# Kernel optimization log

Hardware: AMD Instinct MI355X
Metric: run time of the kernel (lower is better)

The kernel has to match this reference:

```python
import jax, jax.numpy as jnp
import numpy as np

B, N, C = 128, 512, 512  # batch, num_proposals, hidden_dim
K = 3                    # kernel_size
EPS = 1e-5               # LayerNorm eps (torch default)


def setup_inputs() -> dict:
    key = jax.random.key(0)
    k1, k2, k3, k4 = jax.random.split(key, 4)
    query = jax.random.normal(k1, (B, N, C), dtype=jnp.float32)
    value = jax.random.normal(k2, (B, N, C), dtype=jnp.float32)
    # nn.Linear(C, N+K): store transposed weight [C, N+K] for x @ W
    lim = 1.0 / np.sqrt(C)
    W_lin = jax.random.uniform(k3, (C, N + K), minval=-lim, maxval=lim, dtype=jnp.float32)
    b_lin = jax.random.uniform(k4, (N + K,), minval=-lim, maxval=lim, dtype=jnp.float32)
    gamma = jnp.ones((C,), dtype=jnp.float32)
    beta = jnp.zeros((C,), dtype=jnp.float32)
    return {"query": query, "value": value, "W_lin": W_lin, "b_lin": b_lin,
            "gamma": gamma, "beta": beta}


def reference(query, value, W_lin, b_lin, gamma, beta):
    # dynamic weights: [B, N, N+K]
    dy = jnp.einsum('bnc,ck->bnk', query, W_lin) + b_lin
    dw = dy[..., :K]          # depthwise kernel  [B, N, 3]
    pw = dy[..., K:]          # pointwise weights [B, N(out), N(in)]
    # depthwise conv1d along C, groups=N, padding='same' (cross-correlation)
    vp = jnp.pad(value, ((0, 0), (0, 0), (1, 1)))
    depth = (dw[..., 0:1] * vp[..., 0:C]
             + dw[..., 1:2] * vp[..., 1:C + 1]
             + dw[..., 2:3] * vp[..., 2:C + 2])
    depth = jax.nn.relu(depth)
    # pointwise (1x1) conv across proposals: out[b,m,c] = sum_n pw[b,m,n] * depth[b,n,c]
    out = jnp.einsum('bmn,bnc->bmc', pw, depth)
    # LayerNorm over last dim C
    mu = jnp.mean(out, axis=-1, keepdims=True)
    var = jnp.mean(jnp.square(out - mu), axis=-1, keepdims=True)
    return (out - mu) * jax.lax.rsqrt(var + EPS) * gamma + beta
```

## Files before the change

### kernel.cpp

```cpp
#include <hip/hip_runtime.h>
#include <hip/hip_bf16.h>

typedef unsigned short u16;
typedef unsigned int u32;
typedef __attribute__((ext_vector_type(8))) short short8;
typedef __attribute__((ext_vector_type(8))) unsigned short ushort8;
typedef __attribute__((ext_vector_type(4))) float f32x4;

#define AS1 __attribute__((address_space(1)))
#define AS3 __attribute__((address_space(3)))

#define Bb_ 128
#define Nn_ 512
#define Cc_ 512
#define NK_ 515

__device__ __forceinline__ u16 f2bf(float f) {
    union { float f; u32 i; } t; t.f = f;
    u32 x = t.i;
    u32 r = (x + 0x7fffu + ((x >> 16) & 1u)) >> 16;
    return (u16)r;
}

#define ROWS_PER_WAVE 32
__global__ void prep_kernel(const float* __restrict__ q, const float* __restrict__ W,
                            const float* __restrict__ bl,
                            u16* __restrict__ qbf, float* __restrict__ dw) {
    __shared__ float wc[3][512];
    int tid = threadIdx.x;
    for (int idx = tid; idx < 3 * 512; idx += 256) {
        int j = idx >> 9, c = idx & 511;
        wc[j][c] = W[c * NK_ + j];
    }
    __syncthreads();

    int w = tid >> 6, l = tid & 63;
    int c0 = l * 8;
    float w0[8], w1[8], w2[8];
#pragma unroll
    for (int e = 0; e < 8; e++) {
        w0[e] = wc[0][c0 + e];
        w1[e] = wc[1][c0 + e];
        w2[e] = wc[2][c0 + e];
    }
    float bl0 = bl[0], bl1 = bl[1], bl2 = bl[2];

    size_t row0 = (size_t)blockIdx.x * (4 * ROWS_PER_WAVE) + (size_t)w * ROWS_PER_WAVE;
#pragma unroll 2
    for (int rr = 0; rr < ROWS_PER_WAVE; rr++) {
        size_t row = row0 + rr;
        const float* qr = q + row * Cc_;
        f32x4 x0 = *(const f32x4*)(qr + c0);
        f32x4 x1 = *(const f32x4*)(qr + c0 + 4);
        float xf[8] = {x0[0], x0[1], x0[2], x0[3], x1[0], x1[1], x1[2], x1[3]};
        ushort8 y;
        float s0 = 0.f, s1 = 0.f, s2 = 0.f;
#pragma unroll
        for (int e = 0; e < 8; e++) {
            float qf = xf[e];
            y[e] = f2bf(qf);
            s0 += qf * w0[e];
            s1 += qf * w1[e];
            s2 += qf * w2[e];
        }
        *(ushort8*)(qbf + row * Cc_ + c0) = y;
#pragma unroll
        for (int off = 32; off > 0; off >>= 1) {
            s0 += __shfl_xor(s0, off);
            s1 += __shfl_xor(s1, off);
            s2 += __shfl_xor(s2, off);
        }
        if (l == 0) {
            dw[row * 3 + 0] = s0 + bl0;
            dw[row * 3 + 1] = s1 + bl1;
            dw[row * 3 + 2] = s2 + bl2;
        }
    }
}

__global__ void wt_kernel(const float* __restrict__ W, u16* __restrict__ WT) {
    int n = blockIdx.y;
    int c = blockIdx.x * 256 + threadIdx.x;
    WT[n * Cc_ + c] = f2bf(W[c * NK_ + n + 3]);
}

__global__ void depthT_kernel(const float* __restrict__ val, const float* __restrict__ dw,
                              u16* __restrict__ dT) {
    __shared__ float vt[64][67];
    __shared__ float dws[64][3];
    int b = blockIdx.z;
    int c0 = blockIdx.x * 64;
    int n0 = blockIdx.y * 64;
    int tid = threadIdx.x;

    const float* vbase = val + ((size_t)b * Nn_ + n0) * Cc_;
    for (int idx = tid; idx < 64 * 66; idx += 256) {
        int r = idx / 66, cc = idx % 66;
        int c = c0 - 1 + cc;
        float x = 0.f;
        if (c >= 0 && c < Cc_) x = vbase[(size_t)r * Cc_ + c];
        vt[r][cc] = x;
    }
    if (tid < 192) {
        int r = tid / 3, j = tid % 3;
        dws[r][j] = dw[((size_t)b * Nn_ + n0 + r) * 3 + j];
    }
    __syncthreads();

    int nn = tid & 63;
    int ccb = tid >> 6;
    u16* out = dT + ((size_t)b * Cc_ + c0) * Nn_ + n0;
    float d0 = dws[nn][0], d1 = dws[nn][1], d2 = dws[nn][2];
#pragma unroll
    for (int p = 0; p < 16; p++) {
        int cc = ccb + p * 4;
        float x = d0 * vt[nn][cc] + d1 * vt[nn][cc + 1] + d2 * vt[nn][cc + 2];
        x = x > 0.f ? x : 0.f;
        out[(size_t)cc * Nn_ + nn] = f2bf(x);
    }
}

template <int BIAS, int F32OUT>
__global__ __launch_bounds__(256, 2) void gemm_bt(const u16* __restrict__ A,
                                                  const u16* __restrict__ Bt,
                                                  void* __restrict__ Outv,
                                                  const float* __restrict__ bias,
                                                  long sA, long sB, long sO) {
    __shared__ __align__(16) u16 lA[128 * 32];
    __shared__ __align__(16) u16 lB[128 * 32];

    int b = blockIdx.y;
    int tileM = blockIdx.x >> 2;
    int tileN = blockIdx.x & 3;
    const u16* Ab = A + (size_t)b * sA + (size_t)tileM * 128 * 512;
    const u16* Bbp = Bt + (size_t)b * sB + (size_t)tileN * 128 * 512;

    int tid = threadIdx.x, w = tid >> 6, l = tid & 63;
    int rsub = l >> 2;
    int csub = l & 3;
    int wm = w & 1, wn = w >> 1;
    int m_off = wm * 64, n_off = wn * 64;
    int row_l = l & 15, quad = l >> 4;

    f32x4 acc[4][4];
#pragma unroll
    for (int i = 0; i < 4; i++)
#pragma unroll
        for (int j = 0; j < 4; j++) acc[i][j] = (f32x4){0.f, 0.f, 0.f, 0.f};

    for (int kt = 0; kt < 16; kt++) {
        __syncthreads();
        int kof = kt * 32;
#pragma unroll
        for (int j = 0; j < 2; j++) {
            int seg = w * 2 + j;
            int r = seg * 16 + rsub;
            const u16* gA = Ab + (size_t)r * 512 + kof + csub * 8;
            __builtin_amdgcn_global_load_lds((const AS1 u32*)gA,
                                             (AS3 u32*)&lA[seg * 512], 16, 0, 0);
            const u16* gB = Bbp + (size_t)r * 512 + kof + csub * 8;
            __builtin_amdgcn_global_load_lds((const AS1 u32*)gB,
                                             (AS3 u32*)&lB[seg * 512], 16, 0, 0);
        }
        __syncthreads();

        short8 aF[4], bF[4];
#pragma unroll
        for (int i = 0; i < 4; i++)
            aF[i] = *(const short8*)&lA[(m_off + i * 16 + row_l) * 32 + quad * 8];
#pragma unroll
        for (int j = 0; j < 4; j++)
            bF[j] = *(const short8*)&lB[(n_off + j * 16 + row_l) * 32 + quad * 8];

#pragma unroll
        for (int i = 0; i < 4; i++)
#pragma unroll
            for (int j = 0; j < 4; j++)
                acc[i][j] = __builtin_amdgcn_mfma_f32_16x16x32_bf16(aF[i], bF[j], acc[i][j], 0, 0, 0);
    }

#pragma unroll
    for (int i = 0; i < 4; i++) {
#pragma unroll
        for (int j = 0; j < 4; j++) {
            int gn = n_off + j * 16 + row_l;
            float bv = 0.f;
            if (BIAS) bv = bias[tileN * 128 + gn];
#pragma unroll
            for (int r = 0; r < 4; r++) {
                int gm = m_off + i * 16 + quad * 4 + r;
                float vv = acc[i][j][r] + bv;
                size_t idx = (size_t)b * sO + (size_t)tileM * 128 * 512 + tileN * 128 +
                             (size_t)gm * 512 + gn;
                if (F32OUT) ((float*)Outv)[idx] = vv;
                else        ((u16*)Outv)[idx] = f2bf(vv);
            }
        }
    }
}

__global__ void ln_kernel(float* __restrict__ out, const float* __restrict__ gamma,
                          const float* __restrict__ beta) {
    int tid = threadIdx.x, w = tid >> 6, l = tid & 63;
    size_t row = (size_t)blockIdx.x * 4 + w;
    float* p = out + row * Cc_ + l * 8;
    f32x4 x0 = *(const f32x4*)p;
    f32x4 x1 = *(const f32x4*)(p + 4);
    float xf[8] = {x0[0], x0[1], x0[2], x0[3], x1[0], x1[1], x1[2], x1[3]};
    float s = 0.f, ss = 0.f;
#pragma unroll
    for (int e = 0; e < 8; e++) {
        s += xf[e];
        ss += xf[e] * xf[e];
    }
#pragma unroll
    for (int off = 32; off > 0; off >>= 1) {
        s += __shfl_xor(s, off);
        ss += __shfl_xor(ss, off);
    }
    float mu = s * (1.f / 512.f);
    float var = ss * (1.f / 512.f) - mu * mu;
    float rs = rsqrtf(var + 1e-5f);
    f32x4 g0 = *(const f32x4*)(gamma + l * 8);
    f32x4 g1 = *(const f32x4*)(gamma + l * 8 + 4);
    f32x4 b0 = *(const f32x4*)(beta + l * 8);
    f32x4 b1 = *(const f32x4*)(beta + l * 8 + 4);
    float gf[8] = {g0[0], g0[1], g0[2], g0[3], g1[0], g1[1], g1[2], g1[3]};
    float bf[8] = {b0[0], b0[1], b0[2], b0[3], b1[0], b1[1], b1[2], b1[3]};
    f32x4 y0, y1;
#pragma unroll
    for (int e = 0; e < 8; e++) {
        float v = (xf[e] - mu) * rs * gf[e] + bf[e];
        if (e < 4) y0[e] = v; else y1[e - 4] = v;
    }
    *(f32x4*)p = y0;
    *(f32x4*)(p + 4) = y1;
}

extern "C" void kernel_launch(void* const* d_in, const int* in_sizes, int n_in,
                              void* d_out, int out_size, void* d_ws, size_t ws_size,
                              hipStream_t stream) {
    const float* q     = (const float*)d_in[0];
    const float* v     = (const float*)d_in[1];
    const float* W     = (const float*)d_in[2];
    const float* bl    = (const float*)d_in[3];
    const float* gamma = (const float*)d_in[4];
    const float* beta  = (const float*)d_in[5];

    char* ws = (char*)d_ws;
    u16*   WT  = (u16*)ws;
    float* dw  = (float*)(ws + 524288);
    u16*   pw  = (u16*)(ws + 1310720);
    u16*   dT  = (u16*)(ws + 68419584);
    float* out = (float*)d_out;
    u16*   qbf = (u16*)d_out;

    prep_kernel<<<dim3((Bb_ * Nn_) / (4 * ROWS_PER_WAVE)), 256, 0, stream>>>(q, W, bl, qbf, dw);
    wt_kernel<<<dim3(2, 512), 256, 0, stream>>>(W, WT);
    depthT_kernel<<<dim3(8, 8, Bb_), 256, 0, stream>>>(v, dw, dT);

    gemm_bt<1, 0><<<dim3(16, Bb_), 256, 0, stream>>>(qbf, WT, pw, bl + 3,
                                                     (long)Nn_ * Cc_, 0L, (long)Nn_ * Nn_);
    gemm_bt<0, 1><<<dim3(16, Bb_), 256, 0, stream>>>(pw, dT, out, nullptr,
                                                     (long)Nn_ * Nn_, (long)Cc_ * Nn_, (long)Nn_ * Cc_);

    ln_kernel<<<dim3((Bb_ * Nn_) / 4), 256, 0, stream>>>(out, gamma, beta);
}
```

Measured before the change: 546.7 us.

## Fuse LayerNorm into second GEMM, double-buffer LDS, XCD-aware block mapping

Replaces the templated batched GEMM with two specialised kernels. The second GEMM now computes full 64x512 output rows per block, so LayerNorm statistics can be reduced in-block and the separate LN pass (a full fp32 read and write of the output) is removed. Both GEMMs double-buffer the LDS staging so the next k-tile loads overlap with MFMA work, and they remap block IDs so that each XCD handles a contiguous set of batches for L2 locality. The cost is larger LDS use per block (about 72KB for gemm2), a 512-thread block, and higher register pressure, which may reduce occupancy.

New measurement: 510.2 us. 1.07x faster.

```diff
diff --git a/kernel.cpp b/kernel.cpp
--- a/kernel.cpp
+++ b/kernel.cpp
@@ -120,20 +120,21 @@
     }
 }
 
-template <int BIAS, int F32OUT>
-__global__ __launch_bounds__(256, 2) void gemm_bt(const u16* __restrict__ A,
-                                                  const u16* __restrict__ Bt,
-                                                  void* __restrict__ Outv,
-                                                  const float* __restrict__ bias,
-                                                  long sA, long sB, long sO) {
-    __shared__ __align__(16) u16 lA[128 * 32];
-    __shared__ __align__(16) u16 lB[128 * 32];
-
-    int b = blockIdx.y;
-    int tileM = blockIdx.x >> 2;
-    int tileN = blockIdx.x & 3;
-    const u16* Ab = A + (size_t)b * sA + (size_t)tileM * 128 * 512;
-    const u16* Bbp = Bt + (size_t)b * sB + (size_t)tileN * 128 * 512;
+__global__ __launch_bounds__(256, 2) void gemm1(const u16* __restrict__ A,
+                                                const u16* __restrict__ Bt,
+                                                u16* __restrict__ Out,
+                                                const float* __restrict__ bias) {
+    __shared__ __align__(16) u16 lA[2][128 * 32];
+    __shared__ __align__(16) u16 lB[2][128 * 32];
+
+    int wg = blockIdx.x;
+    int xcd = wg & 7, slot = wg >> 3;
+    int b = xcd * 16 + (slot >> 4);
+    int tile = slot & 15;
+    int tileM = tile >> 2, tileN = tile & 3;
+
+    const u16* Ab = A + ((size_t)b * Nn_ + (size_t)tileM * 128) * Cc_;
+    const u16* Bb = Bt + (size_t)tileN * 128 * Cc_;
 
     int tid = threadIdx.x, w = tid >> 6, l = tid & 63;
     int rsub = l >> 2;
@@ -148,35 +149,43 @@
 #pragma unroll
         for (int j = 0; j < 4; j++) acc[i][j] = (f32x4){0.f, 0.f, 0.f, 0.f};
 
-    for (int kt = 0; kt < 16; kt++) {
-        __syncthreads();
+    auto STAGE = [&](int buf, int kt) {
         int kof = kt * 32;
 #pragma unroll
         for (int j = 0; j < 2; j++) {
             int seg = w * 2 + j;
             int r = seg * 16 + rsub;
-            const u16* gA = Ab + (size_t)r * 512 + kof + csub * 8;
+            const u16* gA = Ab + (size_t)r * Cc_ + kof + csub * 8;
             __builtin_amdgcn_global_load_lds((const AS1 u32*)gA,
-                                             (AS3 u32*)&lA[seg * 512], 16, 0, 0);
-            const u16* gB = Bbp + (size_t)r * 512 + kof + csub * 8;
+                                             (AS3 u32*)&lA[buf][seg * 512], 16, 0, 0);
+            const u16* gB = Bb + (size_t)r * Cc_ + kof + csub * 8;
             __builtin_amdgcn_global_load_lds((const AS1 u32*)gB,
-                                             (AS3 u32*)&lB[seg * 512], 16, 0, 0);
-        }
-        __syncthreads();
+                                             (AS3 u32*)&lB[buf][seg * 512], 16, 0, 0);
+        }
+    };
+
+    STAGE(0, 0);
+    __syncthreads();
+    int cur = 0;
+    for (int kt = 0; kt < 16; kt++) {
+        if (kt < 15) STAGE(cur ^ 1, kt + 1);
 
         short8 aF[4], bF[4];
 #pragma unroll
         for (int i = 0; i < 4; i++)
-            aF[i] = *(const short8*)&lA[(m_off + i * 16 + row_l) * 32 + quad * 8];
+            aF[i] = *(const short8*)&lA[cur][(m_off + i * 16 + row_l) * 32 + quad * 8];
 #pragma unroll
         for (int j = 0; j < 4; j++)
-            bF[j] = *(const short8*)&lB[(n_off + j * 16 + row_l) * 32 + quad * 8];
+            bF[j] = *(const short8*)&lB[cur][(n_off + j * 16 + row_l) * 32 + quad * 8];
 
 #pragma unroll
         for (int i = 0; i < 4; i++)
 #pragma unroll
             for (int j = 0; j < 4; j++)
                 acc[i][j] = __builtin_amdgcn_mfma_f32_16x16x32_bf16(aF[i], bF[j], acc[i][j], 0, 0, 0);
+
+        __syncthreads();
+        cur ^= 1;
     }
 
 #pragma unroll
@@ -184,57 +193,143 @@
 #pragma unroll
         for (int j = 0; j < 4; j++) {
             int gn = n_off + j * 16 + row_l;
-            float bv = 0.f;
-            if (BIAS) bv = bias[tileN * 128 + gn];
+            float bv = bias[tileN * 128 + gn];
 #pragma unroll
             for (int r = 0; r < 4; r++) {
                 int gm = m_off + i * 16 + quad * 4 + r;
-                float vv = acc[i][j][r] + bv;
-                size_t idx = (size_t)b * sO + (size_t)tileM * 128 * 512 + tileN * 128 +
-                             (size_t)gm * 512 + gn;
-                if (F32OUT) ((float*)Outv)[idx] = vv;
-                else        ((u16*)Outv)[idx] = f2bf(vv);
+                size_t idx = (size_t)b * Nn_ * Nn_ + (size_t)tileM * 128 * Nn_ +
+                             (size_t)tileN * 128 + (size_t)gm * Nn_ + gn;
+                Out[idx] = f2bf(acc[i][j][r] + bv);
             }
         }
     }
 }
 
-__global__ void ln_kernel(float* __restrict__ out, const float* __restrict__ gamma,
-                          const float* __restrict__ beta) {
+__global__ __launch_bounds__(512, 4) void gemm2_ln(const u16* __restrict__ A,
+                                                   const u16* __restrict__ Bt,
+                                                   float* __restrict__ out,
+                                                   const float* __restrict__ gamma,
+                                                   const float* __restrict__ beta) {
+    __shared__ __align__(16) u16 lA[2][64 * 32];
+    __shared__ __align__(16) u16 lB[2][512 * 32];
+
+    int wg = blockIdx.x;
+    int xcd = wg & 7, slot = wg >> 3;
+    int b = xcd * 16 + (slot >> 3);
+    int tm = slot & 7;
+
+    const u16* Ab = A + ((size_t)b * Nn_ + (size_t)tm * 64) * Nn_;
+    const u16* Bb = Bt + (size_t)b * Cc_ * Nn_;
+
     int tid = threadIdx.x, w = tid >> 6, l = tid & 63;
-    size_t row = (size_t)blockIdx.x * 4 + w;
-    float* p = out + row * Cc_ + l * 8;
-    f32x4 x0 = *(const f32x4*)p;
-    f32x4 x1 = *(const f32x4*)(p + 4);
-    float xf[8] = {x0[0], x0[1], x0[2], x0[3], x1[0], x1[1], x1[2], x1[3]};
-    float s = 0.f, ss = 0.f;
-#pragma unroll
-    for (int e = 0; e < 8; e++) {
-        s += xf[e];
-        ss += xf[e] * xf[e];
-    }
-#pragma unroll
-    for (int off = 32; off > 0; off >>= 1) {
-        s += __shfl_xor(s, off);
-        ss += __shfl_xor(ss, off);
-    }
-    float mu = s * (1.f / 512.f);
-    float var = ss * (1.f / 512.f) - mu * mu;
-    float rs = rsqrtf(var + 1e-5f);
-    f32x4 g0 = *(const f32x4*)(gamma + l * 8);
-    f32x4 g1 = *(const f32x4*)(gamma + l * 8 + 4);
-    f32x4 b0 = *(const f32x4*)(beta + l * 8);
-    f32x4 b1 = *(const f32x4*)(beta + l * 8 + 4);
-    float gf[8] = {g0[0], g0[1], g0[2], g0[3], g1[0], g1[1], g1[2], g1[3]};
-    float bf[8] = {b0[0], b0[1], b0[2], b0[3], b1[0], b1[1], b1[2], b1[3]};
-    f32x4 y0, y1;
-#pragma unroll
-    for (int e = 0; e < 8; e++) {
-        float v = (xf[e] - mu) * rs * gf[e] + bf[e];
-        if (e < 4) y0[e] = v; else y1[e - 4] = v;
-    }
-    *(f32x4*)p = y0;
-    *(f32x4*)(p + 4) = y1;
+    int rsub = l >> 2, csub = l & 3;
+    int row_l = l & 15, quad = l >> 4;
+    int n_off = w * 64;
+
+    f32x4 acc[4][4];
+#pragma unroll
+    for (int i = 0; i < 4; i++)
+#pragma unroll
+        for (int j = 0; j < 4; j++) acc[i][j] = (f32x4){0.f, 0.f, 0.f, 0.f};
+
+    auto STAGE = [&](int buf, int kt) {
+        int kof = kt * 32;
+#pragma unroll
+        for (int j = 0; j < 4; j++) {
+            int seg = w * 4 + j;
+            int r = seg * 16 + rsub;
+            const u16* gB = Bb + (size_t)r * Nn_ + kof + csub * 8;
+            __builtin_amdgcn_global_load_lds((const AS1 u32*)gB,
+                                             (AS3 u32*)&lB[buf][seg * 512], 16, 0, 0);
+        }
+        if (w < 4) {
+            int r = w * 16 + rsub;
+            const u16* gA = Ab + (size_t)r * Nn_ + kof + csub * 8;
+            __builtin_amdgcn_global_load_lds((const AS1 u32*)gA,
+                                             (AS3 u32*)&lA[buf][w * 512], 16, 0, 0);
+        }
+    };
+
+    STAGE(0, 0);
+    __syncthreads();
+    int cur = 0;
+    for (int kt = 0; kt < 16; kt++) {
+        if (kt < 15) STAGE(cur ^ 1, kt + 1);
+
+        short8 aF[4], bF[4];
+#pragma unroll
+        for (int i = 0; i < 4; i++)
+            aF[i] = *(const short8*)&lA[cur][(i * 16 + row_l) * 32 + quad * 8];
+#pragma unroll
+        for (int j = 0; j < 4; j++)
+            bF[j] = *(const short8*)&lB[cur][(n_off + j * 16 + row_l) * 32 + quad * 8];
+
+#pragma unroll
+        for (int i = 0; i < 4; i++)
+#pragma unroll
+            for (int j = 0; j < 4; j++)
+                acc[i][j] = __builtin_amdgcn_mfma_f32_16x16x32_bf16(aF[i], bF[j], acc[i][j], 0, 0, 0);
+
+        __syncthreads();
+        cur ^= 1;
+    }
+
+    float* red  = (float*)&lA[0][0];
+    float* musd = (float*)&lB[0][0];
+
+#pragma unroll
+    for (int i = 0; i < 4; i++) {
+#pragma unroll
+        for (int r = 0; r < 4; r++) {
+            float a0 = acc[i][0][r], a1 = acc[i][1][r], a2 = acc[i][2][r], a3 = acc[i][3][r];
+            float s  = a0 + a1 + a2 + a3;
+            float ss = a0 * a0 + a1 * a1 + a2 * a2 + a3 * a3;
+#pragma unroll
+            for (int off = 8; off > 0; off >>= 1) {
+                s  += __shfl_xor(s, off);
+                ss += __shfl_xor(ss, off);
+            }
+            if (row_l == 0) {
+                int row = i * 16 + quad * 4 + r;
+                red[(w * 64 + row) * 2 + 0] = s;
+                red[(w * 64 + row) * 2 + 1] = ss;
+            }
+        }
+    }
+    __syncthreads();
+    if (w == 0) {
+        float s = 0.f, ss = 0.f;
+#pragma unroll
+        for (int ww = 0; ww < 8; ww++) {
+            s  += red[(ww * 64 + l) * 2 + 0];
+            ss += red[(ww * 64 + l) * 2 + 1];
+        }
+        float mu = s * (1.f / 512.f);
+        float var = ss * (1.f / 512.f) - mu * mu;
+        musd[l] = mu;
+        musd[64 + l] = rsqrtf(var + 1e-5f);
+    }
+    __syncthreads();
+
+    float* outb = out + ((size_t)b * Nn_ + (size_t)tm * 64) * Cc_;
+    int gc0 = n_off + row_l;
+    float gv[4], bv[4];
+#pragma unroll
+    for (int j = 0; j < 4; j++) {
+        gv[j] = gamma[gc0 + j * 16];
+        bv[j] = beta[gc0 + j * 16];
+    }
+#pragma unroll
+    for (int i = 0; i < 4; i++) {
+#pragma unroll
+        for (int r = 0; r < 4; r++) {
+            int row = i * 16 + quad * 4 + r;
+            float mu = musd[row], rs = musd[64 + row];
+#pragma unroll
+            for (int j = 0; j < 4; j++)
+                outb[(size_t)row * Cc_ + gc0 + j * 16] = (acc[i][j][r] - mu) * rs * gv[j] + bv[j];
+        }
+    }
 }
 
 extern "C" void kernel_launch(void* const* d_in, const int* in_sizes, int n_in,
@@ -259,10 +354,6 @@
     wt_kernel<<<dim3(2, 512), 256, 0, stream>>>(W, WT);
     depthT_kernel<<<dim3(8, 8, Bb_), 256, 0, stream>>>(v, dw, dT);
 
-    gemm_bt<1, 0><<<dim3(16, Bb_), 256, 0, stream>>>(qbf, WT, pw, bl + 3,
-                                                     (long)Nn_ * Cc_, 0L, (long)Nn_ * Nn_);
-    gemm_bt<0, 1><<<dim3(16, Bb_), 256, 0, stream>>>(pw, dT, out, nullptr,
-                                                     (long)Nn_ * Nn_, (long)Cc_ * Nn_, (long)Nn_ * Cc_);
-
-    ln_kernel<<<dim3((Bb_ * Nn_) / 4), 256, 0, stream>>>(out, gamma, beta);
-}
+    gemm1<<<dim3(2048), 256, 0, stream>>>(qbf, WT, pw, bl + 3);
+    gemm2_ln<<<dim3(1024), 512, 0, stream>>>(pw, dT, out, gamma, beta);
+}
```
